# Optimization experiments

Measured on AMD Instinct MI355X. Metric: run time of the kernel, lower is better.

## Reference

```python
import jax, jax.numpy as jnp
import numpy as np

B, S, D = 8, 2048, 512          # batch, seq_len, latent_doc_dim
E = 512                          # embedding_dim (== latent_doc_dim here by construction)
NUM_CATS, NUM_LABELS = 1024, 8192
EMB_SCALING = 1.0


def _norm_embed(m, scaling):
    # __init__ preprocessing: m -= m.mean(); m /= m.std() * scaling
    m = m - m.mean()
    return m / (m.std() * scaling)


def setup_inputs() -> dict:
    key = jax.random.key(0)
    k1, k2, k3, k4, k5, k6, k7 = jax.random.split(key, 7)
    K = jax.random.normal(k1, (B, S, D), dtype=jnp.float32)
    V = jax.random.normal(k2, (B, S, D), dtype=jnp.float32)
    code2cat_map = jax.random.randint(k3, (NUM_LABELS,), 0, NUM_CATS)
    # pretrained embedding matrices, normalized as in __init__
    Q1_w = _norm_embed(jax.random.normal(k4, (NUM_CATS, E), dtype=jnp.float32), EMB_SCALING)
    Q2_w = _norm_embed(jax.random.normal(k5, (NUM_LABELS, E), dtype=jnp.float32), EMB_SCALING)
    # Conv1d(kernel_size=1): weight [D_out=latent, D_in=embed], bias [latent]
    map_w = jax.random.normal(k6, (D, E), dtype=jnp.float32) / np.sqrt(E)
    map_b = jax.random.normal(k7, (D,), dtype=jnp.float32) * 0.01
    return {"K": K, "V": V, "code2cat_map": code2cat_map,
            "Q1_w": Q1_w, "Q2_w": Q2_w, "map_w": map_w, "map_b": map_b}


def reference(K, V, code2cat_map, Q1_w, Q2_w, map_w, map_b):
    # kernel-size-1 Conv1d mapping == affine projection of each row embedding
    Q1 = jnp.einsum('ce,de->cd', Q1_w, map_w) + map_b        # [num_cats, D]
    Q2 = jnp.einsum('le,de->ld', Q2_w, map_w) + map_b        # [num_labels, D]
    # level-1 attention (scale=False)
    E1 = jnp.einsum('cd,bsd->bcs', Q1, K)                    # [B, num_cats, S]
    A1 = jax.nn.softmax(E1, axis=-1)
    C1 = jnp.einsum('bcs,bsd->bcd', A1, V)                   # [B, num_cats, D]
    # inject level-1 context into level-2 queries via code->category gather-add
    Q2b = Q2[None, :, :] + C1[:, code2cat_map, :]            # [B, num_labels, D]
    # level-2 attention
    E2 = jnp.einsum('bld,bsd->bls', Q2b, K)                  # [B, num_labels, S]
    A2 = jax.nn.softmax(E2, axis=-1)
    C2 = jnp.einsum('bls,bsd->bld', A2, V)                   # [B, num_labels, D]
    return (C2, E2)
```

## Files before the change

kernel.cpp:

```cpp
#include <hip/hip_runtime.h>
#include <hip/hip_bf16.h>
#include <stdint.h>

#define BB 8
#define SS 2048
#define DD 512
#define NCAT 1024
#define NLAB 8192

typedef short bf16x8 __attribute__((ext_vector_type(8)));
typedef short bf16x4_t __attribute__((ext_vector_type(4)));
typedef float f32x4 __attribute__((ext_vector_type(4)));

__device__ __forceinline__ unsigned short f2bf(float f) {
  union { float f; unsigned int u; } v; v.f = f;
  unsigned int u = v.u;
  return (unsigned short)((u + 0x7fffu + ((u >> 16) & 1u)) >> 16);
}
__device__ __forceinline__ float bf2f(unsigned short h) {
  union { unsigned int u; float f; } v; v.u = ((unsigned int)h) << 16;
  return v.f;
}

__device__ __forceinline__ void gload_lds16(const void* g, void* l) {
  __builtin_amdgcn_global_load_lds(
      (const __attribute__((address_space(1))) unsigned int*)g,
      (__attribute__((address_space(3))) unsigned int*)l, 16, 0, 0);
}

__global__ __launch_bounds__(512, 2) void gemm_e2(
    const short* __restrict__ A,
    const short* __restrict__ Bm,
    float* __restrict__ E2, float* __restrict__ pm, float* __restrict__ ps)
{
  __shared__ __align__(16) char lds[3 * 32768];
  const int t = threadIdx.x;
  const int w = t >> 6, lane = t & 63;
  const int r = lane & 15, g = lane >> 4;
  const int wm = w >> 2, wn = w & 3;
  const int m0 = blockIdx.x * 256, n0 = blockIdx.y * 256;
  const int b = blockIdx.z;
  const short* Ab = A + (long)b * NLAB * DD;
  const short* Bb = Bm + (long)b * SS * DD;

  int offA[8], offB[4];
#pragma unroll
  for (int i = 0; i < 8; ++i) {
    int row = wm * 128 + i * 16 + r;
    int grp = row >> 1, slot = ((row & 1) << 2) | g;
    offA[i] = grp * 128 + (slot ^ (grp & 7)) * 16;
  }
#pragma unroll
  for (int j = 0; j < 4; ++j) {
    int row = wn * 64 + j * 16 + r;
    int grp = row >> 1, slot = ((row & 1) << 2) | g;
    offB[j] = grp * 128 + (slot ^ (grp & 7)) * 16;
  }

  int srow[2], scol[2];
#pragma unroll
  for (int ld = 0; ld < 2; ++ld) {
    int ch = ld * 512 + t;
    int grp = ch >> 3, sl2 = (ch & 7) ^ (grp & 7);
    srow[ld] = grp * 2 + (sl2 >> 2);
    scol[ld] = (sl2 & 3) * 8;
  }

  auto stageA = [&](int kt, int buf) {
    const long kb = (long)(kt * 32);
#pragma unroll
    for (int ld = 0; ld < 2; ++ld)
      gload_lds16(Ab + (long)(m0 + srow[ld]) * DD + kb + scol[ld],
                  lds + buf * 32768 + (ld * 512 + t) * 16);
  };
  auto stageB = [&](int kt, int buf) {
    const long kb = (long)(kt * 32);
#pragma unroll
    for (int ld = 0; ld < 2; ++ld)
      gload_lds16(Bb + (long)(n0 + srow[ld]) * DD + kb + scol[ld],
                  lds + buf * 32768 + 16384 + (ld * 512 + t) * 16);
  };

  f32x4 acc[8][4] = {};

  stageA(0, 0); stageB(0, 0);
  stageA(1, 1); stageB(1, 1);
  asm volatile("s_waitcnt vmcnt(4)" ::: "memory");
  __builtin_amdgcn_s_barrier();
  asm volatile("" ::: "memory");

  int cur = 0;
#pragma unroll 1
  for (int kt = 0; kt < 16; ++kt) {
    if (kt) {
      if (kt == 15) asm volatile("s_waitcnt vmcnt(0)" ::: "memory");
      else          asm volatile("s_waitcnt vmcnt(4)" ::: "memory");
      __builtin_amdgcn_s_barrier();
      asm volatile("" ::: "memory");
    }
    const char* bA = lds + cur * 32768;
    const char* bB = bA + 16384;
    const int nxt = (cur == 0) ? 2 : cur - 1;

    bf16x8 av[4], bv[4];
#pragma unroll
    for (int j = 0; j < 4; ++j) bv[j] = *(const bf16x8*)(bB + offB[j]);
#pragma unroll
    for (int i = 0; i < 4; ++i) av[i] = *(const bf16x8*)(bA + offA[i]);
    if (kt + 2 < 16) stageA(kt + 2, nxt);
    __builtin_amdgcn_s_setprio(1);
#pragma unroll
    for (int i = 0; i < 4; ++i)
#pragma unroll
      for (int j = 0; j < 4; ++j)
        acc[i][j] = __builtin_amdgcn_mfma_f32_16x16x32_bf16(av[i], bv[j], acc[i][j], 0, 0, 0);
    __builtin_amdgcn_s_setprio(0);

#pragma unroll
    for (int i = 0; i < 4; ++i) av[i] = *(const bf16x8*)(bA + offA[4 + i]);
    if (kt + 2 < 16) stageB(kt + 2, nxt);
    __builtin_amdgcn_s_setprio(1);
#pragma unroll
    for (int i = 0; i < 4; ++i)
#pragma unroll
      for (int j = 0; j < 4; ++j)
        acc[4 + i][j] = __builtin_amdgcn_mfma_f32_16x16x32_bf16(av[i], bv[j], acc[4 + i][j], 0, 0, 0);
    __builtin_amdgcn_s_setprio(0);

    cur = (cur == 2) ? 0 : cur + 1;
  }

  float* Cg = E2 + (long)b * NLAB * SS;
#pragma unroll
  for (int i = 0; i < 8; ++i)
#pragma unroll
    for (int j = 0; j < 4; ++j) {
      const int col = n0 + wn * 64 + j * 16 + r;
#pragma unroll
      for (int q = 0; q < 4; ++q) {
        const int row = m0 + wm * 128 + i * 16 + g * 4 + q;
        Cg[(long)row * SS + col] = acc[i][j][q];
      }
    }

  asm volatile("" ::: "memory");
  __builtin_amdgcn_s_barrier();
  asm volatile("" ::: "memory");

  float* smax = (float*)lds;
  float* ssum = (float*)(lds + 4096);
#pragma unroll
  for (int i = 0; i < 8; ++i)
#pragma unroll
    for (int q = 0; q < 4; ++q) {
      float mm = fmaxf(fmaxf(acc[i][0][q], acc[i][1][q]),
                       fmaxf(acc[i][2][q], acc[i][3][q]));
#pragma unroll
      for (int off = 1; off <= 8; off <<= 1) mm = fmaxf(mm, __shfl_xor(mm, off, 64));
      float s = 0.f;
#pragma unroll
      for (int j = 0; j < 4; ++j) s += __expf(acc[i][j][q] - mm);
#pragma unroll
      for (int off = 1; off <= 8; off <<= 1) s += __shfl_xor(s, off, 64);
      if (r == 0) {
        const int rowt = wm * 128 + i * 16 + g * 4 + q;
        smax[rowt * 4 + wn] = mm;
        ssum[rowt * 4 + wn] = s;
      }
    }
  asm volatile("" ::: "memory");
  __builtin_amdgcn_s_barrier();
  asm volatile("" ::: "memory");
  if (t < 256) {
    float m0_ = smax[t * 4 + 0], m1_ = smax[t * 4 + 1];
    float m2_ = smax[t * 4 + 2], m3_ = smax[t * 4 + 3];
    float mm = fmaxf(fmaxf(m0_, m1_), fmaxf(m2_, m3_));
    float s = ssum[t * 4 + 0] * __expf(m0_ - mm) + ssum[t * 4 + 1] * __expf(m1_ - mm)
            + ssum[t * 4 + 2] * __expf(m2_ - mm) + ssum[t * 4 + 3] * __expf(m3_ - mm);
    const long base = ((long)b * NLAB + m0 + t) * 8 + (n0 >> 8);
    pm[base] = mm;
    ps[base] = s;
  }
}

template<int BIAS, int TERMS>
__global__ __launch_bounds__(256) void gemm_nt_split(
    const short* __restrict__ Ah, const short* __restrict__ Al,
    const short* __restrict__ Bh, const short* __restrict__ Bl,
    float* __restrict__ C, const float* __restrict__ bias,
    int M, int N, int K, long sA, long sB, long sC)
{
  __shared__ short AsH[128 * 32];
  __shared__ short AsL[TERMS == 3 ? 128 * 32 : 8];
  __shared__ short BsH[128 * 32];
  __shared__ short BsL[TERMS == 3 ? 128 * 32 : 8];
  const int t = threadIdx.x, w = t >> 6, l = t & 63;
  const int r = l & 15, g = l >> 4;
  const int m0 = blockIdx.x * 128, n0 = blockIdx.y * 128;
  const int b = blockIdx.z;
  const short* Ahb = Ah + (long)b * sA;
  const short* Alb = TERMS == 3 ? Al + (long)b * sA : (const short*)0;
  const short* Bhb = Bh + (long)b * sB;
  const short* Blb = TERMS == 3 ? Bl + (long)b * sB : (const short*)0;
  float* Cg = C + (long)b * sC;
  const int wm = (w >> 1) * 64, wn = (w & 1) * 64;
  const int srow = t >> 2, scol = (t & 3) * 8;

  f32x4 acc[4][4] = {};

  const int nk = K >> 5;
  for (int kt = 0; kt < nk; ++kt) {
    const long k0 = (long)(kt << 5);
    const long ga0 = (long)(m0 + srow) * K + k0 + scol;
    const long ga1 = (long)(m0 + srow + 64) * K + k0 + scol;
    const long gb0 = (long)(n0 + srow) * K + k0 + scol;
    const long gb1 = (long)(n0 + srow + 64) * K + k0 + scol;
    gload_lds16(Ahb + ga0, &AsH[w * 512]);
    gload_lds16(Ahb + ga1, &AsH[2048 + w * 512]);
    gload_lds16(Bhb + gb0, &BsH[w * 512]);
    gload_lds16(Bhb + gb1, &BsH[2048 + w * 512]);
    if (TERMS == 3) {
      gload_lds16(Alb + ga0, &AsL[w * 512]);
      gload_lds16(Alb + ga1, &AsL[2048 + w * 512]);
      gload_lds16(Blb + gb0, &BsL[w * 512]);
      gload_lds16(Blb + gb1, &BsL[2048 + w * 512]);
    }
    __syncthreads();
    bf16x8 ah[4], al_[4], bh[4], bl_[4];
#pragma unroll
    for (int i = 0; i < 4; ++i) {
      ah[i]  = *(const bf16x8*)&AsH[(wm + i * 16 + r) * 32 + g * 8];
      bh[i]  = *(const bf16x8*)&BsH[(wn + i * 16 + r) * 32 + g * 8];
      if (TERMS == 3) {
        al_[i] = *(const bf16x8*)&AsL[(wm + i * 16 + r) * 32 + g * 8];
        bl_[i] = *(const bf16x8*)&BsL[(wn + i * 16 + r) * 32 + g * 8];
      }
    }
#pragma unroll
    for (int i = 0; i < 4; ++i)
#pragma unroll
      for (int j = 0; j < 4; ++j) {
        if (TERMS == 3) {
          acc[i][j] = __builtin_amdgcn_mfma_f32_16x16x32_bf16(al_[i], bh[j], acc[i][j], 0, 0, 0);
          acc[i][j] = __builtin_amdgcn_mfma_f32_16x16x32_bf16(ah[i], bl_[j], acc[i][j], 0, 0, 0);
        }
        acc[i][j] = __builtin_amdgcn_mfma_f32_16x16x32_bf16(ah[i], bh[j], acc[i][j], 0, 0, 0);
      }
    __syncthreads();
  }

#pragma unroll
  for (int i = 0; i < 4; ++i)
#pragma unroll
    for (int j = 0; j < 4; ++j) {
      f32x4 v = acc[i][j];
      const int col = n0 + wn + j * 16 + r;
      float bv = 0.f;
      if (BIAS) bv = bias[col];
#pragma unroll
      for (int q = 0; q < 4; ++q) {
        const int row = m0 + wm + i * 16 + g * 4 + q;
        Cg[(long)row * N + col] = v[q] + bv;
      }
    }
}

__global__ __launch_bounds__(256) void stats_combine(
    const float* __restrict__ pm, const float* __restrict__ ps,
    float2* __restrict__ stats)
{
  const long row = (long)blockIdx.x * 256 + threadIdx.x;
  const float* m = pm + row * 8;
  const float* s = ps + row * 8;
  float mv[8];
  float mm = -3.4e38f;
#pragma unroll
  for (int j = 0; j < 8; ++j) { mv[j] = m[j]; mm = fmaxf(mm, mv[j]); }
  float ss = 0.f;
#pragma unroll
  for (int j = 0; j < 8; ++j) ss += s[j] * __expf(mv[j] - mm);
  stats[row] = make_float2(mm, 1.f / ss);
}

__global__ __launch_bounds__(256) void gemm_c2(
    const float* __restrict__ E2, const float2* __restrict__ stats,
    const short* __restrict__ VT, float* __restrict__ C2)
{
  __shared__ short As[128 * 32];
  __shared__ short Bs[128 * 32];
  const int t = threadIdx.x, w = t >> 6, l = t & 63;
  const int r = l & 15, g = l >> 4;
  const int m0 = blockIdx.x * 128, n0 = blockIdx.y * 128;
  const int b = blockIdx.z;
  const float* Eb = E2 + (long)b * NLAB * SS;
  const float2* sb = stats + (long)b * NLAB;
  const short* Bb = VT + (long)b * DD * SS;
  float* Cg = C2 + (long)b * NLAB * DD;
  const int wm = (w >> 1) * 64, wn = (w & 1) * 64;
  const int srow = t >> 2, scol = (t & 3) * 8;
  const int arow = t >> 3, acol = (t & 7) * 4;

  f32x4 acc[4][4] = {};

  for (int kt = 0; kt < (SS >> 5); ++kt) {
    const int k0 = kt << 5;
    gload_lds16(Bb + (long)(n0 + srow) * SS + k0 + scol, &Bs[w * 512]);
    gload_lds16(Bb + (long)(n0 + srow + 64) * SS + k0 + scol, &Bs[2048 + w * 512]);
#pragma unroll
    for (int it = 0; it < 4; ++it) {
      const int row = it * 32 + arow;
      f32x4 e = *(const f32x4*)(Eb + (long)(m0 + row) * SS + k0 + acol);
      float2 st = sb[m0 + row];
      bf16x4_t p;
#pragma unroll
      for (int q = 0; q < 4; ++q) p[q] = (short)f2bf(__expf(e[q] - st.x) * st.y);
      *(bf16x4_t*)&As[row * 32 + acol] = p;
    }
    __syncthreads();
    bf16x8 af[4], bfr[4];
#pragma unroll
    for (int i = 0; i < 4; ++i) {
      af[i]  = *(const bf16x8*)&As[(wm + i * 16 + r) * 32 + g * 8];
      bfr[i] = *(const bf16x8*)&Bs[(wn + i * 16 + r) * 32 + g * 8];
    }
#pragma unroll
    for (int i = 0; i < 4; ++i)
#pragma unroll
      for (int j = 0; j < 4; ++j)
        acc[i][j] = __builtin_amdgcn_mfma_f32_16x16x32_bf16(af[i], bfr[j], acc[i][j], 0, 0, 0);
    __syncthreads();
  }

#pragma unroll
  for (int i = 0; i < 4; ++i)
#pragma unroll
    for (int j = 0; j < 4; ++j) {
      f32x4 v = acc[i][j];
      const int col = n0 + wn + j * 16 + r;
#pragma unroll
      for (int q = 0; q < 4; ++q)
        Cg[(long)(m0 + wm + i * 16 + g * 4 + q) * DD + col] = v[q];
    }
}

__global__ __launch_bounds__(256) void rowsoft_p(
    const float* __restrict__ X, short* __restrict__ Ph)
{
  __shared__ float red[8];
  const long row = blockIdx.x;
  const float* x = X + row * SS;
  const int t = threadIdx.x, w = t >> 6;
  f32x4 v0 = *(const f32x4*)(x + t * 4);
  f32x4 v1 = *(const f32x4*)(x + 1024 + t * 4);
  float m = fmaxf(fmaxf(fmaxf(v0[0], v0[1]), fmaxf(v0[2], v0[3])),
                  fmaxf(fmaxf(v1[0], v1[1]), fmaxf(v1[2], v1[3])));
#pragma unroll
  for (int off = 32; off; off >>= 1) m = fmaxf(m, __shfl_xor(m, off, 64));
  if ((t & 63) == 0) red[w] = m;
  __syncthreads();
  m = fmaxf(fmaxf(red[0], red[1]), fmaxf(red[2], red[3]));
  float s = 0.f;
#pragma unroll
  for (int i = 0; i < 4; ++i) { v0[i] = __expf(v0[i] - m); s += v0[i]; }
#pragma unroll
  for (int i = 0; i < 4; ++i) { v1[i] = __expf(v1[i] - m); s += v1[i]; }
#pragma unroll
  for (int off = 32; off; off >>= 1) s += __shfl_xor(s, off, 64);
  if ((t & 63) == 0) red[4 + w] = s;
  __syncthreads();
  s = red[4] + red[5] + red[6] + red[7];
  const float inv = 1.f / s;
  bf16x4_t h0, h1;
#pragma unroll
  for (int i = 0; i < 4; ++i) {
    h0[i] = (short)f2bf(v0[i] * inv);
    h1[i] = (short)f2bf(v1[i] * inv);
  }
  *(bf16x4_t*)(Ph + row * SS + t * 4) = h0;
  *(bf16x4_t*)(Ph + row * SS + 1024 + t * 4) = h1;
}

__global__ __launch_bounds__(256) void cvt_split(
    const float* __restrict__ in, short* __restrict__ hi, short* __restrict__ lo, long n4)
{
  long i = (long)blockIdx.x * 256 + threadIdx.x;
  const long stride = (long)gridDim.x * 256;
  for (; i < n4; i += stride) {
    f32x4 v = *(const f32x4*)(in + i * 4);
    bf16x4_t h, lw;
#pragma unroll
    for (int q = 0; q < 4; ++q) {
      h[q] = (short)f2bf(v[q]);
      lw[q] = (short)f2bf(v[q] - bf2f((unsigned short)h[q]));
    }
    *(bf16x4_t*)(hi + i * 4) = h;
    *(bf16x4_t*)(lo + i * 4) = lw;
  }
}

__global__ __launch_bounds__(256) void vtrans(
    const float* __restrict__ V, short* __restrict__ TH)
{
  __shared__ float tile[32][33];
  const int b = blockIdx.z;
  const int s0 = blockIdx.x * 32, d0 = blockIdx.y * 32;
  const int tx = threadIdx.x & 31, ty = threadIdx.x >> 5;
  const float* Vb = V + (long)b * SS * DD;
  short* Hb = TH + (long)b * DD * SS;
#pragma unroll
  for (int i = 0; i < 32; i += 8)
    tile[ty + i][tx] = Vb[(long)(s0 + ty + i) * DD + d0 + tx];
  __syncthreads();
#pragma unroll
  for (int i = 0; i < 32; i += 8)
    Hb[(long)(d0 + ty + i) * SS + s0 + tx] = (short)f2bf(tile[tx][ty + i]);
}

__global__ __launch_bounds__(256) void make_q2b(
    const float* __restrict__ Q2f, const float* __restrict__ C1,
    const int* __restrict__ map, short* __restrict__ Oh)
{
  const long idx = (long)blockIdx.x * 256 + threadIdx.x;
  const long per_b = (long)NLAB * (DD / 4);
  const int b = (int)(idx / per_b);
  const long rem = idx - (long)b * per_b;
  const int ll = (int)(rem >> 7);
  const int dd = (int)(rem & 127) << 2;
  const int cat = map[ll];
  f32x4 qv = *(const f32x4*)(Q2f + (long)ll * DD + dd);
  f32x4 cv = *(const f32x4*)(C1 + ((long)b * NCAT + cat) * DD + dd);
  bf16x4_t h;
#pragma unroll
  for (int q = 0; q < 4; ++q) h[q] = (short)f2bf(qv[q] + cv[q]);
  *(bf16x4_t*)(Oh + idx * 4) = h;
}

extern "C" void kernel_launch(void* const* d_in, const int* in_sizes, int n_in,
                              void* d_out, int out_size, void* d_ws, size_t ws_size,
                              hipStream_t stream)
{
  const float* K    = (const float*)d_in[0];
  const float* V    = (const float*)d_in[1];
  const int*   map  = (const int*)d_in[2];
  const float* Q1w  = (const float*)d_in[3];
  const float* Q2w  = (const float*)d_in[4];
  const float* mapw = (const float*)d_in[5];
  const float* mapb = (const float*)d_in[6];

  float* out = (float*)d_out;
  const long C2SZ = (long)BB * NLAB * DD;
  float* outC2 = out;
  float* outE2 = out + C2SZ;

  char* ws = (char*)d_ws;
  short* Kh   = (short*)ws; ws += (long)BB * SS * DD * 2;
  short* Kl   = (short*)ws; ws += (long)BB * SS * DD * 2;
  short* VTh  = (short*)ws; ws += (long)BB * DD * SS * 2;
  short* Qwh  = (short*)ws; ws += (long)(NCAT + NLAB) * DD * 2;
  short* Qwl  = (short*)ws; ws += (long)(NCAT + NLAB) * DD * 2;
  short* mwh  = (short*)ws; ws += (long)DD * DD * 2;
  short* mwl  = (short*)ws; ws += (long)DD * DD * 2;
  float* Qall = (float*)ws; ws += (long)(NCAT + NLAB) * DD * 4;
  short* A1h  = (short*)ws; ws += (long)BB * NCAT * SS * 2;
  float* C1   = (float*)ws; ws += (long)BB * NCAT * DD * 4;
  short* Q2bh = (short*)ws; ws += (long)BB * NLAB * DD * 2;
  float* pm   = (float*)ws; ws += (long)BB * NLAB * 8 * 4;
  float* psum = (float*)ws; ws += (long)BB * NLAB * 8 * 4;
  float2* stats = (float2*)ws;

  cvt_split<<<2048, 256, 0, stream>>>(K, Kh, Kl, (long)BB * SS * DD / 4);
  vtrans<<<dim3(SS / 32, DD / 32, BB), 256, 0, stream>>>(V, VTh);
  cvt_split<<<512, 256, 0, stream>>>(Q1w, Qwh, Qwl, (long)NCAT * DD / 4);
  cvt_split<<<2048, 256, 0, stream>>>(Q2w, Qwh + (long)NCAT * DD, Qwl + (long)NCAT * DD,
                                      (long)NLAB * DD / 4);
  cvt_split<<<256, 256, 0, stream>>>(mapw, mwh, mwl, (long)DD * DD / 4);

  gemm_nt_split<1, 3><<<dim3((NCAT + NLAB) / 128, DD / 128, 1), 256, 0, stream>>>(
      Qwh, Qwl, mwh, mwl, Qall, mapb, NCAT + NLAB, DD, DD, 0, 0, 0);

  cvt_split<<<2048, 256, 0, stream>>>(Qall, Qwh, Qwl, (long)(NCAT + NLAB) * DD / 4);

  gemm_nt_split<0, 3><<<dim3(NCAT / 128, SS / 128, BB), 256, 0, stream>>>(
      Qwh, Qwl, Kh, Kl, outE2, (const float*)0,
      NCAT, SS, DD, 0, (long)SS * DD, (long)NCAT * SS);

  rowsoft_p<<<BB * NCAT, 256, 0, stream>>>(outE2, A1h);

  gemm_nt_split<0, 1><<<dim3(NCAT / 128, DD / 128, BB), 256, 0, stream>>>(
      A1h, (const short*)0, VTh, (const short*)0, C1, (const float*)0,
      NCAT, DD, SS, (long)NCAT * SS, (long)DD * SS, (long)NCAT * DD);

  make_q2b<<<(int)((long)BB * NLAB * DD / 4 / 256), 256, 0, stream>>>(
      Qall + (long)NCAT * DD, C1, map, Q2bh);

  gemm_e2<<<dim3(NLAB / 256, SS / 256, BB), 512, 0, stream>>>(
      Q2bh, Kh, outE2, pm, psum);

  stats_combine<<<BB * NLAB / 256, 256, 0, stream>>>(pm, psum, stats);

  gemm_c2<<<dim3(NLAB / 128, DD / 128, BB), 256, 0, stream>>>(
      outE2, stats, VTh, outC2);
}
```

Before: 860.1 us.

## Rewrite C2 GEMM with 256x256 tiles, triple-buffered LDS and register prefetch

```diff
diff --git a/kernel.cpp b/kernel.cpp
--- a/kernel.cpp
+++ b/kernel.cpp
@@ -181,6 +181,148 @@
     pm[base] = mm;
     ps[base] = s;
   }
+}
+
+__global__ __launch_bounds__(512, 2) void gemm_c2p(
+    const float* __restrict__ E2, const float2* __restrict__ stats,
+    const short* __restrict__ VT, float* __restrict__ C2)
+{
+  __shared__ __align__(16) char lds[3 * 32768];
+  const int t = threadIdx.x;
+  const int w = t >> 6, lane = t & 63;
+  const int r = lane & 15, g = lane >> 4;
+  const int wm = w >> 2, wn = w & 3;
+  const int m0 = blockIdx.x * 256, n0 = blockIdx.y * 256;
+  const int b = blockIdx.z;
+  const float* Eb = E2 + (long)b * NLAB * SS;
+  const short* Bb = VT + (long)b * DD * SS;
+
+  int offA[8], offB[4];
+#pragma unroll
+  for (int i = 0; i < 8; ++i) {
+    int row = wm * 128 + i * 16 + r;
+    int grp = row >> 1, slot = ((row & 1) << 2) | g;
+    offA[i] = grp * 128 + (slot ^ (grp & 7)) * 16;
+  }
+#pragma unroll
+  for (int j = 0; j < 4; ++j) {
+    int row = wn * 64 + j * 16 + r;
+    int grp = row >> 1, slot = ((row & 1) << 2) | g;
+    offB[j] = grp * 128 + (slot ^ (grp & 7)) * 16;
+  }
+
+  int srow[2], scol[2];
+#pragma unroll
+  for (int ld = 0; ld < 2; ++ld) {
+    int ch = ld * 512 + t;
+    int grp = ch >> 3, sl2 = (ch & 7) ^ (grp & 7);
+    srow[ld] = grp * 2 + (sl2 >> 2);
+    scol[ld] = (sl2 & 3) * 8;
+  }
+
+  const int arow = t >> 1;
+  const int ac0 = (t & 1) * 16;
+  int wbyte[2];
+  {
+    const int grp = arow >> 1, cc0 = ac0 >> 3;
+#pragma unroll
+    for (int ld = 0; ld < 2; ++ld) {
+      const int slot = ((arow & 1) << 2) | (cc0 + ld);
+      wbyte[ld] = grp * 128 + (slot ^ (grp & 7)) * 16;
+    }
+  }
+  const float2 st = stats[(long)b * NLAB + m0 + arow];
+  const float* asrc = Eb + (long)(m0 + arow) * SS + ac0;
+
+  float areg[16];
+  auto loadA = [&](int kt) {
+    const float* src = asrc + kt * 32;
+#pragma unroll
+    for (int u = 0; u < 4; ++u)
+      *(f32x4*)(areg + u * 4) = *(const f32x4*)(src + u * 4);
+  };
+  auto writeA = [&](int buf) {
+    char* dst = lds + buf * 32768;
+#pragma unroll
+    for (int ld = 0; ld < 2; ++ld) {
+      bf16x8 p;
+#pragma unroll
+      for (int q = 0; q < 8; ++q)
+        p[q] = (short)f2bf(__expf(areg[ld * 8 + q] - st.x) * st.y);
+      *(bf16x8*)(dst + wbyte[ld]) = p;
+    }
+  };
+  auto stageB = [&](int kt, int buf) {
+    const long kb = (long)(kt * 32);
+#pragma unroll
+    for (int ld = 0; ld < 2; ++ld)
+      gload_lds16(Bb + (long)(n0 + srow[ld]) * SS + kb + scol[ld],
+                  lds + buf * 32768 + 16384 + (ld * 512 + t) * 16);
+  };
+
+  f32x4 acc[8][4] = {};
+
+  loadA(0); stageB(0, 0); writeA(0);
+  loadA(1); stageB(1, 1); writeA(1);
+  asm volatile("s_waitcnt lgkmcnt(0)" ::: "memory");
+  __builtin_amdgcn_s_barrier();
+  asm volatile("" ::: "memory");
+
+  int cur = 0;
+#pragma unroll 1
+  for (int kt = 0; kt < 64; ++kt) {
+    if (kt) {
+      if (kt == 63) asm volatile("s_waitcnt vmcnt(0)" ::: "memory");
+      asm volatile("s_waitcnt lgkmcnt(0)" ::: "memory");
+      __builtin_amdgcn_s_barrier();
+      asm volatile("" ::: "memory");
+    }
+    const char* bA = lds + cur * 32768;
+    const char* bB = bA + 16384;
+    const int nxt = (cur == 0) ? 2 : cur - 1;
+
+    if (kt + 2 < 64) { loadA(kt + 2); stageB(kt + 2, nxt); }
+
+    bf16x8 av[4], bv[4];
+#pragma unroll
+    for (int j = 0; j < 4; ++j) bv[j] = *(const bf16x8*)(bB + offB[j]);
+#pragma unroll
+    for (int i = 0; i < 4; ++i) av[i] = *(const bf16x8*)(bA + offA[i]);
+    __builtin_amdgcn_s_setprio(1);
+#pragma unroll
+    for (int i = 0; i < 4; ++i)
+#pragma unroll
+      for (int j = 0; j < 4; ++j)
+        acc[i][j] = __builtin_amdgcn_mfma_f32_16x16x32_bf16(av[i], bv[j], acc[i][j], 0, 0, 0);
+    __builtin_amdgcn_s_setprio(0);
+
+#pragma unroll
+    for (int i = 0; i < 4; ++i) av[i] = *(const bf16x8*)(bA + offA[4 + i]);
+    __builtin_amdgcn_s_setprio(1);
+#pragma unroll
+    for (int i = 0; i < 4; ++i)
+#pragma unroll
+      for (int j = 0; j < 4; ++j)
+        acc[4 + i][j] = __builtin_amdgcn_mfma_f32_16x16x32_bf16(av[i], bv[j], acc[4 + i][j], 0, 0, 0);
+    __builtin_amdgcn_s_setprio(0);
+
+    if (kt + 2 < 64) writeA(nxt);
+
+    cur = (cur == 2) ? 0 : cur + 1;
+  }
+
+  float* Cg = C2 + (long)b * NLAB * DD;
+#pragma unroll
+  for (int i = 0; i < 8; ++i)
+#pragma unroll
+    for (int j = 0; j < 4; ++j) {
+      const int col = n0 + wn * 64 + j * 16 + r;
+#pragma unroll
+      for (int q = 0; q < 4; ++q) {
+        const int row = m0 + wm * 128 + i * 16 + g * 4 + q;
+        Cg[(long)row * DD + col] = acc[i][j][q];
+      }
+    }
 }
 
 template<int BIAS, int TERMS>
@@ -282,67 +424,6 @@
   stats[row] = make_float2(mm, 1.f / ss);
 }
 
-__global__ __launch_bounds__(256) void gemm_c2(
-    const float* __restrict__ E2, const float2* __restrict__ stats,
-    const short* __restrict__ VT, float* __restrict__ C2)
-{
-  __shared__ short As[128 * 32];
-  __shared__ short Bs[128 * 32];
-  const int t = threadIdx.x, w = t >> 6, l = t & 63;
-  const int r = l & 15, g = l >> 4;
-  const int m0 = blockIdx.x * 128, n0 = blockIdx.y * 128;
-  const int b = blockIdx.z;
-  const float* Eb = E2 + (long)b * NLAB * SS;
-  const float2* sb = stats + (long)b * NLAB;
-  const short* Bb = VT + (long)b * DD * SS;
-  float* Cg = C2 + (long)b * NLAB * DD;
-  const int wm = (w >> 1) * 64, wn = (w & 1) * 64;
-  const int srow = t >> 2, scol = (t & 3) * 8;
-  const int arow = t >> 3, acol = (t & 7) * 4;
-
-  f32x4 acc[4][4] = {};
-
-  for (int kt = 0; kt < (SS >> 5); ++kt) {
-    const int k0 = kt << 5;
-    gload_lds16(Bb + (long)(n0 + srow) * SS + k0 + scol, &Bs[w * 512]);
-    gload_lds16(Bb + (long)(n0 + srow + 64) * SS + k0 + scol, &Bs[2048 + w * 512]);
-#pragma unroll
-    for (int it = 0; it < 4; ++it) {
-      const int row = it * 32 + arow;
-      f32x4 e = *(const f32x4*)(Eb + (long)(m0 + row) * SS + k0 + acol);
-      float2 st = sb[m0 + row];
-      bf16x4_t p;
-#pragma unroll
-      for (int q = 0; q < 4; ++q) p[q] = (short)f2bf(__expf(e[q] - st.x) * st.y);
-      *(bf16x4_t*)&As[row * 32 + acol] = p;
-    }
-    __syncthreads();
-    bf16x8 af[4], bfr[4];
-#pragma unroll
-    for (int i = 0; i < 4; ++i) {
-      af[i]  = *(const bf16x8*)&As[(wm + i * 16 + r) * 32 + g * 8];
-      bfr[i] = *(const bf16x8*)&Bs[(wn + i * 16 + r) * 32 + g * 8];
-    }
-#pragma unroll
-    for (int i = 0; i < 4; ++i)
-#pragma unroll
-      for (int j = 0; j < 4; ++j)
-        acc[i][j] = __builtin_amdgcn_mfma_f32_16x16x32_bf16(af[i], bfr[j], acc[i][j], 0, 0, 0);
-    __syncthreads();
-  }
-
-#pragma unroll
-  for (int i = 0; i < 4; ++i)
-#pragma unroll
-    for (int j = 0; j < 4; ++j) {
-      f32x4 v = acc[i][j];
-      const int col = n0 + wn + j * 16 + r;
-#pragma unroll
-      for (int q = 0; q < 4; ++q)
-        Cg[(long)(m0 + wm + i * 16 + g * 4 + q) * DD + col] = v[q];
-    }
-}
-
 __global__ __launch_bounds__(256) void rowsoft_p(
     const float* __restrict__ X, short* __restrict__ Ph)
 {
@@ -498,6 +579,6 @@
 
   stats_combine<<<BB * NLAB / 256, 256, 0, stream>>>(pm, psum, stats);
 
-  gemm_c2<<<dim3(NLAB / 128, DD / 128, BB), 256, 0, stream>>>(
+  gemm_c2p<<<dim3(NLAB / 256, DD / 256, BB), 512, 0, stream>>>(
       outE2, stats, VTh, outC2);
 }
```

Result: faster. 819.5 us (-4.7%).
